# Kernel optimization log

Hardware: AMD Instinct MI355X
Metric: run time of the kernel (lower is better)

Reference implementation:

```python
import jax, jax.numpy as jnp
import numpy as np

LIMIT = 0.01  # codebook init range, per module's `limit` arg


def setup_inputs() -> dict:
    key = jax.random.key(0)
    k1, k2 = jax.random.split(key)
    B, T, D, K = 64, 1024, 256, 4096
    x = jax.random.normal(k1, (B, T, D), dtype=jnp.float32)
    # codebook: (embedding_dim, num_embeddings), uniform in [-limit, limit]
    vectors = jax.random.uniform(k2, (D, K), dtype=jnp.float32, minval=-LIMIT, maxval=LIMIT)
    return {"x": x, "vectors": vectors}


def reference(x, vectors):
    D = x.shape[-1]
    flat_x = x.reshape(-1, D)  # (N, D)
    # squared euclidean distances to each codebook vector: (N, K)
    distances = ((flat_x ** 2).sum(axis=1, keepdims=True)
                 - 2.0 * flat_x @ vectors
                 + (vectors ** 2).sum(axis=0, keepdims=True))
    encoding_indices = jnp.argmin(distances, axis=1)  # (N,)
    # gather nearest codebook vectors: vectors.T is (K, D)
    quantized_x = jnp.take(vectors.T, encoding_indices, axis=0).reshape(x.shape)
    dictionary_loss = jnp.mean((jax.lax.stop_gradient(x) - quantized_x) ** 2)
    commitment_loss = jnp.mean((x - jax.lax.stop_gradient(quantized_x)) ** 2)
    # straight-through estimator
    quantized_st = x + jax.lax.stop_gradient(quantized_x - x)
    return (quantized_st, dictionary_loss, commitment_loss,
            encoding_indices.reshape(x.shape[0], -1))
```

## Files before the change

### kernel.cpp

```cpp
#include <hip/hip_runtime.h>
#include <cfloat>

#define NROWS 65536
#define DIM   256
#define KCB   4096

typedef __attribute__((ext_vector_type(8))) short bf16x8;
typedef __attribute__((ext_vector_type(4))) float f32x4;
typedef unsigned short ushort;
typedef unsigned int uint;


__device__ __forceinline__ bool better(float v1, int i1, float v2, int i2) {
    return (v1 < v2) || (v1 == v2 && i1 < i2);
}

__device__ __forceinline__ float opaque(float x) {
    asm volatile("" : "+v"(x));
    return x;
}

__device__ __forceinline__ ushort f2bf(float f) {
    uint u = __float_as_uint(f);
    return (ushort)((u + 0x7FFFu + ((u >> 16) & 1u)) >> 16);
}

__device__ __forceinline__ void insert4b(float v[4], int idx[4], float s, int k) {
    if (better(s, k, v[3], idx[3])) {
        if (better(s, k, v[2], idx[2])) {
            v[3] = v[2]; idx[3] = idx[2];
            if (better(s, k, v[1], idx[1])) {
                v[2] = v[1]; idx[2] = idx[1];
                if (better(s, k, v[0], idx[0])) {
                    v[1] = v[0]; idx[1] = idx[0]; v[0] = s; idx[0] = k;
                } else { v[1] = s; idx[1] = k; }
            } else { v[2] = s; idx[2] = k; }
        } else { v[3] = s; idx[3] = k; }
    }
}

__global__ void vq_cref_kernel(const float* __restrict__ v,
                               float* __restrict__ cref) {
    int k = blockIdx.x * blockDim.x + threadIdx.x;
    float t = v[k];
    float c = opaque(t * t);
    for (int d = 1; d < DIM; ++d) {
        t = v[d * KCB + k];
        c = c + opaque(t * t);
    }
    cref[k] = c;
}

__global__ void vq_transpose_kernel(const float* __restrict__ v,
                                    float* __restrict__ vt) {
    __shared__ float tile[32][33];
    int d0 = blockIdx.x * 32;
    int k0 = blockIdx.y * 32;
    int tx = threadIdx.x;
    int ty = threadIdx.y;
    #pragma unroll
    for (int i = 0; i < 32; i += 8)
        tile[ty + i][tx] = v[(d0 + ty + i) * KCB + k0 + tx];
    __syncthreads();
    #pragma unroll
    for (int i = 0; i < 32; i += 8)
        vt[(k0 + ty + i) * DIM + d0 + tx] = tile[tx][ty + i];
}

__global__ __launch_bounds__(256) void vq_pack_kernel(const float* __restrict__ vt,
                                                      ushort* __restrict__ vthp) {
    int t = blockIdx.x * 256 + threadIdx.x;
    int lane = t & 63;
    int dt   = (t >> 6) & 7;
    int g    = t >> 9;
    int row  = g * 16 + (lane & 15);
    int dbase = (dt * 4 + (lane >> 4)) * 8;
    const float* src = vt + (size_t)row * DIM + dbase;
    float4 f0 = *(const float4*)src;
    float4 f1 = *(const float4*)(src + 4);
    int4 p;
    p.x = (int)f2bf(f0.x) | ((int)f2bf(f0.y) << 16);
    p.y = (int)f2bf(f0.z) | ((int)f2bf(f0.w) << 16);
    p.z = (int)f2bf(f1.x) | ((int)f2bf(f1.y) << 16);
    p.w = (int)f2bf(f1.z) | ((int)f2bf(f1.w) << 16);
    *(int4*)(vthp + (size_t)t * 8) = p;
}

__global__ __launch_bounds__(256, 4) void vq_mfma_argmin_kernel(
        const float* __restrict__ x, const ushort* __restrict__ vthp,
        const float* __restrict__ cref, int4* __restrict__ cand) {
    __shared__ __align__(16) ushort Bk[32 * 64 * 8];

    const int tid  = threadIdx.x;
    const int w    = tid >> 6;
    const int lane = tid & 63;
    const int l15  = lane & 15;
    const int quad = lane >> 4;
    const int row0 = blockIdx.x * 64;

    {
        const int r_ = tid >> 2;
        const int q_ = tid & 3;
        const float* xs = &x[(size_t)(row0 + r_) * DIM + q_ * 64];
        #pragma unroll
        for (int i = 0; i < 8; ++i) {
            float4 f0 = *(const float4*)(xs + i * 8);
            float4 f1 = *(const float4*)(xs + i * 8 + 4);
            int4 p;
            p.x = (int)f2bf(f0.x) | ((int)f2bf(f0.y) << 16);
            p.y = (int)f2bf(f0.z) | ((int)f2bf(f0.w) << 16);
            p.z = (int)f2bf(f1.x) | ((int)f2bf(f1.y) << 16);
            p.w = (int)f2bf(f1.z) | ((int)f2bf(f1.w) << 16);
            int u = q_ * 8 + i;
            *(int4*)&Bk[(u * 64 + r_) * 8] = p;
        }
    }
    __syncthreads();

    float m0[4], m1[4];
    #pragma unroll
    for (int nj = 0; nj < 4; ++nj) { m0[nj] = FLT_MAX; m1[nj] = FLT_MAX; }

    for (int kt = 0; kt < 16; ++kt) {
        f32x4 acc[4][4];
        #pragma unroll
        for (int mi = 0; mi < 4; ++mi)
            #pragma unroll
            for (int nj = 0; nj < 4; ++nj)
                acc[mi][nj] = (f32x4)0.f;

        const ushort* akt = vthp
            + ((size_t)(kt * 16 + w * 4) * 8 * 64 + lane) * 8;

        #pragma unroll 2
        for (int dt = 0; dt < 8; ++dt) {
            bf16x8 af[4], bfr[4];
            #pragma unroll
            for (int mi = 0; mi < 4; ++mi)
                af[mi] = *(const bf16x8*)(akt + mi * 4096 + dt * 512);
            #pragma unroll
            for (int nj = 0; nj < 4; ++nj)
                bfr[nj] = *(const bf16x8*)&Bk[((dt * 4 + quad) * 64 + nj * 16 + l15) * 8];
            #pragma unroll
            for (int mi = 0; mi < 4; ++mi)
                #pragma unroll
                for (int nj = 0; nj < 4; ++nj)
                    acc[mi][nj] = __builtin_amdgcn_mfma_f32_16x16x32_bf16(
                        af[mi], bfr[nj], acc[mi][nj], 0, 0, 0);
        }

        const uint ktb = (uint)(kt << 4);
        float4 cv[4];
        #pragma unroll
        for (int mi = 0; mi < 4; ++mi)
            cv[mi] = *(const float4*)&cref[kt * 256 + w * 64 + mi * 16 + quad * 4];

        #pragma unroll
        for (int nj = 0; nj < 4; ++nj) {
            #pragma unroll
            for (int mi = 0; mi < 4; ++mi) {
                #pragma unroll
                for (int r = 0; r < 4; ++r) {
                    float s = fmaf(-2.f, acc[mi][nj][r], (&cv[mi].x)[r]);
                    uint  pk = (__float_as_uint(s) & 0xFFFFFF00u)
                             | (ktb + (uint)(mi * 4 + r));
                    float f = __uint_as_float(pk);
                    m1[nj] = __builtin_amdgcn_fmed3f(f, m0[nj], m1[nj]);
                    m0[nj] = fminf(m0[nj], f);
                }
            }
        }
    }

    float mv[4][4];
    int   mi_[4][4];
    #pragma unroll
    for (int nj = 0; nj < 4; ++nj) {
        uint b0 = __float_as_uint(m0[nj]);
        uint b1 = __float_as_uint(m1[nj]);
        int id0 = (int)(b0 & 255u);
        int id1 = (int)(b1 & 255u);
        mv[nj][0] = m0[nj];
        mi_[nj][0] = ((id0 >> 4) << 8) + w * 64 + (((id0 >> 2) & 3) << 4)
                   + (quad << 2) + (id0 & 3);
        mv[nj][1] = m1[nj];
        mi_[nj][1] = ((id1 >> 4) << 8) + w * 64 + (((id1 >> 2) & 3) << 4)
                   + (quad << 2) + (id1 & 3);
        mv[nj][2] = FLT_MAX; mi_[nj][2] = 0;
        mv[nj][3] = FLT_MAX; mi_[nj][3] = 0;
    }
    #pragma unroll
    for (int off = 16; off <= 32; off <<= 1) {
        #pragma unroll
        for (int nj = 0; nj < 4; ++nj) {
            float ov[4]; int oi[4];
            #pragma unroll
            for (int s = 0; s < 4; ++s) {
                ov[s] = __shfl_xor(mv[nj][s], off);
                oi[s] = __shfl_xor(mi_[nj][s], off);
            }
            #pragma unroll
            for (int s = 0; s < 4; ++s)
                insert4b(mv[nj], mi_[nj], ov[s], oi[s]);
        }
    }

    __syncthreads();
    float2* mbuf = (float2*)Bk;
    if (quad == 0) {
        #pragma unroll
        for (int nj = 0; nj < 4; ++nj) {
            int row_local = nj * 16 + l15;
            #pragma unroll
            for (int s = 0; s < 4; ++s)
                mbuf[row_local * 16 + w * 4 + s] =
                    make_float2(mv[nj][s], __int_as_float(mi_[nj][s]));
        }
    }
    __syncthreads();
    if (tid < 64) {
        float bv[4] = {FLT_MAX, FLT_MAX, FLT_MAX, FLT_MAX};
        int   bi[4] = {0, 0, 0, 0};
        #pragma unroll
        for (int j = 0; j < 16; ++j) {
            float2 p = mbuf[tid * 16 + j];
            insert4b(bv, bi, p.x, __float_as_int(p.y));
        }
        cand[row0 + tid] = make_int4(bi[0], bi[1], bi[2], bi[3]);
    }
}

__global__ __launch_bounds__(256) void vq_emulate_kernel(
        const float* __restrict__ x, const float* __restrict__ vt,
        const float* __restrict__ cref, int4* __restrict__ cand,
        float* __restrict__ out_idx) {
    int gid = blockIdx.x * blockDim.x + threadIdx.x;
    int row = gid >> 2;
    int c   = ((const int*)cand)[gid];

    const float4* xr = (const float4*)(x + (size_t)row * DIM);
    const float4* vr = (const float4*)(vt + (size_t)c * DIM);

    float b = 0.f;
    float A_half[2];
    #pragma unroll
    for (int h = 0; h < 2; ++h) {
        float r[8];
        for (int i = 0; i < 16; ++i) {
            float4 xa = xr[h * 32 + i * 2];
            float4 xb = xr[h * 32 + i * 2 + 1];
            float4 va = vr[h * 32 + i * 2];
            float4 vb = vr[h * 32 + i * 2 + 1];
            float xs[8] = {xa.x, xa.y, xa.z, xa.w, xb.x, xb.y, xb.z, xb.w};
            float vs[8] = {va.x, va.y, va.z, va.w, vb.x, vb.y, vb.z, vb.w};
            if (i == 0) {
                #pragma unroll
                for (int j = 0; j < 8; ++j) {
                    r[j] = opaque(xs[j] * xs[j]);
                    b = fmaf(2.f * xs[j], vs[j], b);
                }
            } else {
                #pragma unroll
                for (int j = 0; j < 8; ++j) {
                    r[j] = r[j] + opaque(xs[j] * xs[j]);
                    b = fmaf(2.f * xs[j], vs[j], b);
                }
            }
        }
        A_half[h] = ((r[0] + r[1]) + (r[2] + r[3])) + ((r[4] + r[5]) + (r[6] + r[7]));
    }
    float A = A_half[0] + A_half[1];

    float bd = (A - b) + cref[c];
    int   bk = c;
    #pragma unroll
    for (int off = 1; off <= 2; off <<= 1) {
        float ov = __shfl_xor(bd, off);
        int   oi = __shfl_xor(bk, off);
        if (better(ov, oi, bd, bk)) { bd = ov; bk = oi; }
    }
    if ((gid & 3) == 0) {
        ((int*)(cand + row))[3] = bk;
        out_idx[row] = (float)bk;
    }
}

__global__ __launch_bounds__(256) void vq_quant_kernel(
        const float* __restrict__ x, const float* __restrict__ vt,
        const int4* __restrict__ cand, float* __restrict__ out_q,
        float* __restrict__ partial) {
    const int tid    = threadIdx.x;
    const int rlocal = tid >> 6;
    const int lane   = tid & 63;
    const int row    = blockIdx.x * 4 + rlocal;
    const int k      = ((const int*)(cand + row))[3];

    float4 xv = *(const float4*)&x[(size_t)row * DIM + lane * 4];
    float4 q  = *(const float4*)&vt[(size_t)k * DIM + lane * 4];
    *(float4*)&out_q[(size_t)row * DIM + lane * 4] = q;

    float dx = xv.x - q.x, dy = xv.y - q.y, dz = xv.z - q.z, dw = xv.w - q.w;
    float sum = dx * dx + dy * dy + dz * dz + dw * dw;
    #pragma unroll
    for (int off = 32; off > 0; off >>= 1)
        sum += __shfl_xor(sum, off);

    __shared__ float bsum[4];
    if (lane == 0) bsum[rlocal] = sum;
    __syncthreads();
    if (tid == 0)
        partial[blockIdx.x] = bsum[0] + bsum[1] + bsum[2] + bsum[3];
}

__global__ void vq_finalize_kernel(const float* __restrict__ partial,
                                   float* __restrict__ out_loss) {
    __shared__ double sd[256];
    double s = 0.0;
    for (int i = threadIdx.x; i < NROWS / 4; i += 256)
        s += (double)partial[i];
    sd[threadIdx.x] = s;
    __syncthreads();
    for (int off = 128; off > 0; off >>= 1) {
        if (threadIdx.x < off) sd[threadIdx.x] += sd[threadIdx.x + off];
        __syncthreads();
    }
    if (threadIdx.x == 0) {
        double m = sd[0] / (double)((long long)NROWS * DIM);
        out_loss[0] = (float)m;
        out_loss[1] = (float)m;
    }
}

extern "C" void kernel_launch(void* const* d_in, const int* in_sizes, int n_in,
                              void* d_out, int out_size, void* d_ws, size_t ws_size,
                              hipStream_t stream) {
    const float* x = (const float*)d_in[0];
    const float* v = (const float*)d_in[1];

    float* out      = (float*)d_out;
    float* out_q    = out;
    float* out_loss = out + (size_t)NROWS * DIM;
    float* out_idx  = out + (size_t)NROWS * DIM + 2;

    char*   ws      = (char*)d_ws;
    float*  cref    = (float*)ws;
    int4*   cand    = (int4*)(ws + 32768);
    float*  partial = (float*)(ws + 1081344);
    float*  vt      = (float*)(ws + 1343488);
    ushort* vthp    = (ushort*)(ws + 5537792);

    vq_cref_kernel<<<KCB / 256, 256, 0, stream>>>(v, cref);
    vq_transpose_kernel<<<dim3(DIM / 32, KCB / 32), dim3(32, 8), 0, stream>>>(v, vt);
    vq_pack_kernel<<<512, 256, 0, stream>>>(vt, vthp);
    vq_mfma_argmin_kernel<<<NROWS / 64, 256, 0, stream>>>(x, vthp, cref, cand);
    vq_emulate_kernel<<<NROWS * 4 / 256, 256, 0, stream>>>(x, vt, cref, cand, out_idx);
    vq_quant_kernel<<<NROWS / 4, 256, 0, stream>>>(x, vt, cand, out_q, partial);
    vq_finalize_kernel<<<1, 256, 0, stream>>>(partial, out_loss);
}
```

Before: 404.9 us.

## Fuse candidate rescoring and quantize/loss into the MFMA argmin kernel

Measured after the change: 418.7 us. 1.03x slower.

```diff
diff --git a/kernel.cpp b/kernel.cpp
--- a/kernel.cpp
+++ b/kernel.cpp
@@ -4,6 +4,7 @@
 #define NROWS 65536
 #define DIM   256
 #define KCB   4096
+#define NBLK  (NROWS / 64)
 
 typedef __attribute__((ext_vector_type(8))) short bf16x8;
 typedef __attribute__((ext_vector_type(4))) float f32x4;
@@ -88,7 +89,9 @@
 
 __global__ __launch_bounds__(256, 4) void vq_mfma_argmin_kernel(
         const float* __restrict__ x, const ushort* __restrict__ vthp,
-        const float* __restrict__ cref, int4* __restrict__ cand) {
+        const float* __restrict__ vt, const float* __restrict__ cref,
+        float* __restrict__ out_q, float* __restrict__ out_idx,
+        float* __restrict__ partial) {
     __shared__ __align__(16) ushort Bk[32 * 64 * 8];
 
     const int tid  = threadIdx.x;
@@ -206,7 +209,10 @@
     }
 
     __syncthreads();
-    float2* mbuf = (float2*)Bk;
+    float2* mbuf  = (float2*)Bk;
+    int*    candL = (int*)(Bk + 8192);
+    int*    kwin  = (int*)(Bk + 8704);
+    float*  rsum  = (float*)(Bk + 8960);
     if (quad == 0) {
         #pragma unroll
         for (int nj = 0; nj < 4; ++nj) {
@@ -226,97 +232,101 @@
             float2 p = mbuf[tid * 16 + j];
             insert4b(bv, bi, p.x, __float_as_int(p.y));
         }
-        cand[row0 + tid] = make_int4(bi[0], bi[1], bi[2], bi[3]);
-    }
-}
-
-__global__ __launch_bounds__(256) void vq_emulate_kernel(
-        const float* __restrict__ x, const float* __restrict__ vt,
-        const float* __restrict__ cref, int4* __restrict__ cand,
-        float* __restrict__ out_idx) {
-    int gid = blockIdx.x * blockDim.x + threadIdx.x;
-    int row = gid >> 2;
-    int c   = ((const int*)cand)[gid];
-
-    const float4* xr = (const float4*)(x + (size_t)row * DIM);
-    const float4* vr = (const float4*)(vt + (size_t)c * DIM);
-
-    float b = 0.f;
-    float A_half[2];
-    #pragma unroll
-    for (int h = 0; h < 2; ++h) {
-        float r[8];
-        for (int i = 0; i < 16; ++i) {
-            float4 xa = xr[h * 32 + i * 2];
-            float4 xb = xr[h * 32 + i * 2 + 1];
-            float4 va = vr[h * 32 + i * 2];
-            float4 vb = vr[h * 32 + i * 2 + 1];
-            float xs[8] = {xa.x, xa.y, xa.z, xa.w, xb.x, xb.y, xb.z, xb.w};
-            float vs[8] = {va.x, va.y, va.z, va.w, vb.x, vb.y, vb.z, vb.w};
-            if (i == 0) {
-                #pragma unroll
-                for (int j = 0; j < 8; ++j) {
-                    r[j] = opaque(xs[j] * xs[j]);
-                    b = fmaf(2.f * xs[j], vs[j], b);
-                }
-            } else {
-                #pragma unroll
-                for (int j = 0; j < 8; ++j) {
-                    r[j] = r[j] + opaque(xs[j] * xs[j]);
-                    b = fmaf(2.f * xs[j], vs[j], b);
+        #pragma unroll
+        for (int s = 0; s < 4; ++s)
+            candL[tid * 4 + s] = bi[s];
+    }
+    __syncthreads();
+
+    {
+        const int row = tid >> 2;
+        const int cl  = tid & 3;
+        const int c   = candL[row * 4 + cl];
+
+        const float4* xr = (const float4*)(x + (size_t)(row0 + row) * DIM);
+        const float4* vr = (const float4*)(vt + (size_t)c * DIM);
+
+        float b = 0.f;
+        float A_half[2];
+        #pragma unroll
+        for (int h = 0; h < 2; ++h) {
+            float r[8];
+            for (int i = 0; i < 16; ++i) {
+                float4 xa = xr[h * 32 + i * 2];
+                float4 xb = xr[h * 32 + i * 2 + 1];
+                float4 va = vr[h * 32 + i * 2];
+                float4 vb = vr[h * 32 + i * 2 + 1];
+                float xs[8] = {xa.x, xa.y, xa.z, xa.w, xb.x, xb.y, xb.z, xb.w};
+                float vs[8] = {va.x, va.y, va.z, va.w, vb.x, vb.y, vb.z, vb.w};
+                if (i == 0) {
+                    #pragma unroll
+                    for (int j = 0; j < 8; ++j) {
+                        r[j] = opaque(xs[j] * xs[j]);
+                        b = fmaf(2.f * xs[j], vs[j], b);
+                    }
+                } else {
+                    #pragma unroll
+                    for (int j = 0; j < 8; ++j) {
+                        r[j] = r[j] + opaque(xs[j] * xs[j]);
+                        b = fmaf(2.f * xs[j], vs[j], b);
+                    }
                 }
             }
-        }
-        A_half[h] = ((r[0] + r[1]) + (r[2] + r[3])) + ((r[4] + r[5]) + (r[6] + r[7]));
-    }
-    float A = A_half[0] + A_half[1];
-
-    float bd = (A - b) + cref[c];
-    int   bk = c;
-    #pragma unroll
-    for (int off = 1; off <= 2; off <<= 1) {
-        float ov = __shfl_xor(bd, off);
-        int   oi = __shfl_xor(bk, off);
-        if (better(ov, oi, bd, bk)) { bd = ov; bk = oi; }
-    }
-    if ((gid & 3) == 0) {
-        ((int*)(cand + row))[3] = bk;
-        out_idx[row] = (float)bk;
-    }
-}
-
-__global__ __launch_bounds__(256) void vq_quant_kernel(
-        const float* __restrict__ x, const float* __restrict__ vt,
-        const int4* __restrict__ cand, float* __restrict__ out_q,
-        float* __restrict__ partial) {
-    const int tid    = threadIdx.x;
-    const int rlocal = tid >> 6;
-    const int lane   = tid & 63;
-    const int row    = blockIdx.x * 4 + rlocal;
-    const int k      = ((const int*)(cand + row))[3];
-
-    float4 xv = *(const float4*)&x[(size_t)row * DIM + lane * 4];
-    float4 q  = *(const float4*)&vt[(size_t)k * DIM + lane * 4];
-    *(float4*)&out_q[(size_t)row * DIM + lane * 4] = q;
-
-    float dx = xv.x - q.x, dy = xv.y - q.y, dz = xv.z - q.z, dw = xv.w - q.w;
-    float sum = dx * dx + dy * dy + dz * dz + dw * dw;
-    #pragma unroll
-    for (int off = 32; off > 0; off >>= 1)
-        sum += __shfl_xor(sum, off);
-
-    __shared__ float bsum[4];
-    if (lane == 0) bsum[rlocal] = sum;
-    __syncthreads();
-    if (tid == 0)
-        partial[blockIdx.x] = bsum[0] + bsum[1] + bsum[2] + bsum[3];
+            A_half[h] = ((r[0] + r[1]) + (r[2] + r[3])) + ((r[4] + r[5]) + (r[6] + r[7]));
+        }
+        float A = A_half[0] + A_half[1];
+
+        float bd = (A - b) + cref[c];
+        int   bk = c;
+        #pragma unroll
+        for (int off = 1; off <= 2; off <<= 1) {
+            float ov = __shfl_xor(bd, off);
+            int   oi = __shfl_xor(bk, off);
+            if (better(ov, oi, bd, bk)) { bd = ov; bk = oi; }
+        }
+        if (cl == 0) {
+            kwin[row] = bk;
+            out_idx[row0 + row] = (float)bk;
+        }
+    }
+    __syncthreads();
+
+    {
+        const int row = tid >> 2;
+        const int cl  = tid & 3;
+        const int k   = kwin[row];
+        const float* xs = x  + (size_t)(row0 + row) * DIM + cl * 64;
+        const float* vs = vt + (size_t)k * DIM + cl * 64;
+        float*       qs = out_q + (size_t)(row0 + row) * DIM + cl * 64;
+        float lsum = 0.f;
+        #pragma unroll
+        for (int i = 0; i < 16; ++i) {
+            float4 xv = *(const float4*)(xs + i * 4);
+            float4 qv = *(const float4*)(vs + i * 4);
+            *(float4*)(qs + i * 4) = qv;
+            float dx = xv.x - qv.x, dy = xv.y - qv.y;
+            float dz = xv.z - qv.z, dw = xv.w - qv.w;
+            lsum += dx * dx + dy * dy + dz * dz + dw * dw;
+        }
+        lsum += __shfl_xor(lsum, 1);
+        lsum += __shfl_xor(lsum, 2);
+        if (cl == 0) rsum[row] = lsum;
+    }
+    __syncthreads();
+    if (tid < 64) {
+        float s = rsum[tid];
+        #pragma unroll
+        for (int off = 32; off > 0; off >>= 1)
+            s += __shfl_xor(s, off);
+        if (tid == 0) partial[blockIdx.x] = s;
+    }
 }
 
 __global__ void vq_finalize_kernel(const float* __restrict__ partial,
                                    float* __restrict__ out_loss) {
     __shared__ double sd[256];
     double s = 0.0;
-    for (int i = threadIdx.x; i < NROWS / 4; i += 256)
+    for (int i = threadIdx.x; i < NBLK; i += 256)
         s += (double)partial[i];
     sd[threadIdx.x] = s;
     __syncthreads();
@@ -344,7 +354,6 @@
 
     char*   ws      = (char*)d_ws;
     float*  cref    = (float*)ws;
-    int4*   cand    = (int4*)(ws + 32768);
     float*  partial = (float*)(ws + 1081344);
     float*  vt      = (float*)(ws + 1343488);
     ushort* vthp    = (ushort*)(ws + 5537792);
@@ -352,8 +361,7 @@
     vq_cref_kernel<<<KCB / 256, 256, 0, stream>>>(v, cref);
     vq_transpose_kernel<<<dim3(DIM / 32, KCB / 32), dim3(32, 8), 0, stream>>>(v, vt);
     vq_pack_kernel<<<512, 256, 0, stream>>>(vt, vthp);
-    vq_mfma_argmin_kernel<<<NROWS / 64, 256, 0, stream>>>(x, vthp, cref, cand);
-    vq_emulate_kernel<<<NROWS * 4 / 256, 256, 0, stream>>>(x, vt, cref, cand, out_idx);
-    vq_quant_kernel<<<NROWS / 4, 256, 0, stream>>>(x, vt, cand, out_q, partial);
+    vq_mfma_argmin_kernel<<<NBLK, 256, 0, stream>>>(x, vthp, vt, cref,
+                                                    out_q, out_idx, partial);
     vq_finalize_kernel<<<1, 256, 0, stream>>>(partial, out_loss);
 }
```
